# Performance work log

Hardware: AMD Instinct MI355X
Metric: run time of the kernel (lower is better)

The kernel has to match this reference:

```python
import jax, jax.numpy as jnp
import numpy as np
import math

B, S, E, H, L, VOCAB, OUT = 32, 1024, 512, 8, 2, 20000, 1
D = E // H


def positional_encoding(seq_length, embed_size):
    position = jnp.arange(seq_length, dtype=jnp.float32)[:, None]
    div_term = jnp.exp(jnp.arange(0, embed_size, 2, dtype=jnp.float32) * (-math.log(10000.0) / embed_size))
    pe = jnp.zeros((seq_length, embed_size), dtype=jnp.float32)
    pe = pe.at[:, 0::2].set(jnp.sin(position * div_term))
    pe = pe.at[:, 1::2].set(jnp.cos(position * div_term))
    return pe


def setup_inputs() -> dict:
    key = jax.random.key(0)
    ks = jax.random.split(key, 12)
    inputs = jax.random.randint(ks[0], (B, S), 0, VOCAB)
    s = 1.0 / math.sqrt(E)
    embed_table = jax.random.normal(ks[1], (VOCAB, E), jnp.float32)
    embed_table = embed_table.at[0].set(0.0)  # padding_idx=0
    # per-layer Q,K,V,O linear weights [L,E,E] (applied as x @ W + b) and biases [L,E]
    Wq = jax.random.normal(ks[2], (L, E, E), jnp.float32) * s
    Wk = jax.random.normal(ks[3], (L, E, E), jnp.float32) * s
    Wv = jax.random.normal(ks[4], (L, E, E), jnp.float32) * s
    Wo = jax.random.normal(ks[5], (L, E, E), jnp.float32) * s
    bq = jax.random.normal(ks[6], (L, E), jnp.float32) * s
    bk = jax.random.normal(ks[7], (L, E), jnp.float32) * s
    bv = jax.random.normal(ks[8], (L, E), jnp.float32) * s
    bo = jax.random.normal(ks[9], (L, E), jnp.float32) * s
    W_out = jax.random.normal(ks[10], (E, OUT), jnp.float32) * s
    b_out = jax.random.normal(ks[11], (OUT,), jnp.float32) * s
    return {"inputs": inputs, "embed_table": embed_table, "Wq": Wq, "bq": bq,
            "Wk": Wk, "bk": bk, "Wv": Wv, "bv": bv, "Wo": Wo, "bo": bo,
            "W_out": W_out, "b_out": b_out}


def _mha(x, Wq, bq, Wk, bk, Wv, bv, Wo, bo, mask):
    b, s = x.shape[:2]
    def heads(W, bias):
        return (x @ W + bias).reshape(b, s, H, D).transpose(0, 2, 1, 3)  # [b,H,s,D]
    q, k, v = heads(Wq, bq), heads(Wk, bk), heads(Wv, bv)
    scores = jnp.einsum('bhqd,bhkd->bhqk', q, k) / math.sqrt(D)
    scores = jnp.where(mask, -1e9, scores)
    prob = jax.nn.softmax(scores, axis=-1)
    out = jnp.einsum('bhqk,bhkd->bhqd', prob, v)
    out = out.transpose(0, 2, 1, 3).reshape(b, s, E)
    return out @ Wo + bo


def reference(inputs, embed_table, Wq, bq, Wk, bk, Wv, bv, Wo, bo, W_out, b_out):
    embeds = embed_table[inputs]  # [B,S,E]
    embeds = embeds + positional_encoding(inputs.shape[1], embeds.shape[-1])
    mask = jnp.triu(jnp.ones((inputs.shape[1], inputs.shape[1]), bool), k=1)  # future mask
    out = embeds
    for l in range(L):
        attn = _mha(out, Wq[l], bq[l], Wk[l], bk[l], Wv[l], bv[l], Wo[l], bo[l], mask)
        out = out + jax.nn.relu(attn)  # dropout is identity (eval / p=0)
    return out @ W_out + b_out
```

## Files before the change

kernel.cpp:

```cpp
#include <hip/hip_runtime.h>

typedef unsigned short u16;
typedef unsigned int u32;
using short8  = __attribute__((ext_vector_type(8))) short;
using floatx4 = __attribute__((ext_vector_type(4))) float;

#define NB 32
#define SEQ 1024
#define EMB 512
#define NH 8
#define HD 64
#define NLAYER 2
#define M_ROWS (NB * SEQ)

__device__ __forceinline__ float bf2f(u16 u) {
  union { u32 i; float f; } v; v.i = ((u32)u) << 16; return v.f;
}
__device__ __forceinline__ u16 f2bf(float f) {
  union { float f; u32 i; } v; v.f = f;
  u32 r = v.i + 0x7fffu + ((v.i >> 16) & 1u);
  return (u16)(r >> 16);
}
__device__ __forceinline__ u32 cvtpk(float a, float b) {
  u32 r;
  asm volatile("v_cvt_pk_bf16_f32 %0, %1, %2" : "=v"(r) : "v"(a), "v"(b));
  return r;
}

#if __has_builtin(__builtin_amdgcn_exp2f)
#define EXP2F __builtin_amdgcn_exp2f
#else
#define EXP2F exp2f
#endif

typedef __attribute__((address_space(3))) unsigned int lds_u32_t;
typedef __attribute__((address_space(1))) const unsigned int gbl_u32_t;
__device__ __forceinline__ void gload16(void* lds, const void* g) {
  gbl_u32_t* gp = (gbl_u32_t*)(unsigned long long)g;
  lds_u32_t* lp = (lds_u32_t*)(unsigned int)(unsigned long long)lds;
  __builtin_amdgcn_global_load_lds(gp, lp, 16, 0, 0);
}

__global__ void prep_weights(const float* __restrict__ Wq, const float* __restrict__ Wk,
                             const float* __restrict__ Wv, const float* __restrict__ Wo,
                             u16* __restrict__ WtQKV, u16* __restrict__ WtO) {
  int idx = blockIdx.x * 256 + threadIdx.x;
  const int QKV_TOT = NLAYER * 3 * EMB * EMB;
  if (idx < QKV_TOT) {
    int l = idx / (3 * EMB * EMB);
    int rem = idx % (3 * EMB * EMB);
    int n = rem / EMB, kk = rem % EMB;
    int w = n >> 9, e = n & 511;
    const float* src = (w == 0) ? Wq : (w == 1) ? Wk : Wv;
    WtQKV[idx] = f2bf(src[((size_t)l * EMB + kk) * EMB + e]);
  } else {
    int j = idx - QKV_TOT;
    int l = j / (EMB * EMB);
    int rem = j % (EMB * EMB);
    int n = rem / EMB, kk = rem % EMB;
    WtO[j] = f2bf(Wo[((size_t)l * EMB + kk) * EMB + n]);
  }
}

__global__ void pe_table(float* __restrict__ pe) {
  int idx = blockIdx.x * 256 + threadIdx.x;
  int s = idx >> 9, e = idx & 511;
  int i = e >> 1;
  const float negln = -9.210340371976184f / (float)EMB;
  float dt = __expf((float)(2 * i) * negln);
  float ang = (float)s * dt;
  pe[idx] = (e & 1) ? __cosf(ang) : __sinf(ang);
}

__global__ void embed_pe(const int* __restrict__ inp, const float* __restrict__ table,
                         const float* __restrict__ pe, u16* __restrict__ x) {
  int row = blockIdx.x;
  int tok = inp[row];
  int s = row & (SEQ - 1);
  int e = threadIdx.x * 2;
  float2 tv = *(const float2*)&table[(size_t)tok * EMB + e];
  float2 pv = *(const float2*)&pe[(size_t)s * EMB + e];
  *(u32*)&x[(size_t)row * EMB + e] = cvtpk(tv.x + pv.x, tv.y + pv.y);
}

#define BK 32

__global__ __launch_bounds__(256) void gemm_bt(
    const u16* __restrict__ A, const u16* __restrict__ Bt, int K, int mode,
    const float* bias0, const float* bias1, const float* bias2,
    u16* out0, u16* out1, u16* out2, const u16* resid, int Nstride) {
  __shared__ u16 sA[3][128][BK];
  __shared__ u16 sB[3][128][BK];
  int tid = threadIdx.x;
  int wave = tid >> 6, lane = tid & 63;
  int quad = lane >> 4, l16 = lane & 15;
  int wm = wave >> 1, wn = wave & 1;

  int NT = (mode == 0) ? 12 : 4;
  int blk = blockIdx.x;
  int xcd = blk & 7, slot = blk >> 3;
  int mtl = slot / NT, ntl = slot % NT;
  int bm0 = (xcd * 32 + mtl) * 128;
  int bn0 = ntl * 128;
  bool vswap = (mode == 0) && (bn0 >= 1024);

  floatx4 acc[4][4];
#pragma unroll
  for (int i = 0; i < 4; ++i)
#pragma unroll
    for (int j = 0; j < 4; ++j) acc[i][j] = (floatx4){0.f, 0.f, 0.f, 0.f};

  int rb = wave * 32;
  int lrow = lane >> 2;
  int gcg = ((lane & 3) ^ ((lane >> 3) & 3)) * 8;
  int rsl = (quad ^ ((l16 >> 1) & 3)) * 8;

  const u16* Arow0 = &A[(size_t)(bm0 + rb + lrow) * K + gcg];
  const u16* Arow1 = &A[(size_t)(bm0 + rb + 16 + lrow) * K + gcg];
  const u16* Brow0 = &Bt[(size_t)(bn0 + rb + lrow) * K + gcg];
  const u16* Brow1 = &Bt[(size_t)(bn0 + rb + 16 + lrow) * K + gcg];

  gload16(&sA[0][rb][0],      Arow0);
  gload16(&sA[0][rb + 16][0], Arow1);
  gload16(&sB[0][rb][0],      Brow0);
  gload16(&sB[0][rb + 16][0], Brow1);
  gload16(&sA[1][rb][0],      Arow0 + BK);
  gload16(&sA[1][rb + 16][0], Arow1 + BK);
  gload16(&sB[1][rb][0],      Brow0 + BK);
  gload16(&sB[1][rb + 16][0], Brow1 + BK);

  const int niter = K / BK;
  int c0 = 0, c1 = 1, c2 = 2;
  for (int it = 0; it < niter; ++it) {
    if (it + 2 < niter) {
      int k2 = (it + 2) * BK;
      gload16(&sA[c2][rb][0],      Arow0 + k2);
      gload16(&sA[c2][rb + 16][0], Arow1 + k2);
      gload16(&sB[c2][rb][0],      Brow0 + k2);
      gload16(&sB[c2][rb + 16][0], Brow1 + k2);
      asm volatile("s_waitcnt vmcnt(8)" ::: "memory");
    } else if (it + 1 < niter) {
      asm volatile("s_waitcnt vmcnt(4)" ::: "memory");
    } else {
      asm volatile("s_waitcnt vmcnt(0)" ::: "memory");
    }
    asm volatile("s_barrier" ::: "memory");

    short8 af[4], bfr[4];
#pragma unroll
    for (int mi = 0; mi < 4; ++mi)
      af[mi] = *(const short8*)&sA[c0][wm * 64 + mi * 16 + l16][rsl];
#pragma unroll
    for (int ni = 0; ni < 4; ++ni)
      bfr[ni] = *(const short8*)&sB[c0][wn * 64 + ni * 16 + l16][rsl];
    if (!vswap) {
#pragma unroll
      for (int mi = 0; mi < 4; ++mi)
#pragma unroll
        for (int ni = 0; ni < 4; ++ni)
          acc[mi][ni] = __builtin_amdgcn_mfma_f32_16x16x32_bf16(af[mi], bfr[ni], acc[mi][ni], 0, 0, 0);
    } else {
#pragma unroll
      for (int mi = 0; mi < 4; ++mi)
#pragma unroll
        for (int ni = 0; ni < 4; ++ni)
          acc[mi][ni] = __builtin_amdgcn_mfma_f32_16x16x32_bf16(bfr[ni], af[mi], acc[mi][ni], 0, 0, 0);
    }
    asm volatile("s_waitcnt lgkmcnt(0)" ::: "memory");
    asm volatile("s_barrier" ::: "memory");
    int t = c0; c0 = c1; c1 = c2; c2 = t;
  }

  u16* scr = ((u16*)sA) + wave * (16 * 68);
  int erow = lane >> 5;
  int dcol = lane & 31;

  if (!vswap) {
    int w = bn0 >> 9;
    const float* bp = (mode == 1) ? bias0 : ((w == 0) ? bias0 : bias1);
    float sc = (mode == 0 && w == 0) ? 0.18033688011112042f : 1.0f;
    float bvs[4];
#pragma unroll
    for (int ni = 0; ni < 4; ++ni)
      bvs[ni] = bp[(bn0 + wn * 64 + ni * 16 + l16) & 511] * sc;

    int colg = bn0 + wn * 64 + dcol * 2;
#pragma unroll
    for (int mi = 0; mi < 4; ++mi) {
#pragma unroll
      for (int ni = 0; ni < 4; ++ni) {
        float t0 = fmaf(acc[mi][ni][0], sc, bvs[ni]);
        float t1 = fmaf(acc[mi][ni][1], sc, bvs[ni]);
        float t2 = fmaf(acc[mi][ni][2], sc, bvs[ni]);
        float t3 = fmaf(acc[mi][ni][3], sc, bvs[ni]);
        if (mode == 1) {
          t0 = fmaxf(t0, 0.f); t1 = fmaxf(t1, 0.f);
          t2 = fmaxf(t2, 0.f); t3 = fmaxf(t3, 0.f);
        }
        u32 p01 = cvtpk(t0, t1), p23 = cvtpk(t2, t3);
        int base = (quad * 4) * 68 + ni * 16 + l16;
        scr[base]       = (u16)p01;
        scr[base + 68]  = (u16)(p01 >> 16);
        scr[base + 136] = (u16)p23;
        scr[base + 204] = (u16)(p23 >> 16);
      }
      asm volatile("s_waitcnt lgkmcnt(0)" ::: "memory");

      int m0 = bm0 + wm * 64 + mi * 16;
      if (mode == 0) {
        int e = colg & 511, hh = e >> 6, dd = e & 63;
        int bb = m0 >> 10, sid0 = m0 & 1023;
        u16* optr = (w == 0) ? out0 : out1;
        u16* op = &optr[((size_t)(bb * NH + hh) * SEQ + sid0) * HD + dd];
#pragma unroll
        for (int p = 0; p < 8; ++p) {
          int row = p * 2 + erow;
          u32 d2 = *(const u32*)&scr[row * 68 + dcol * 2];
          *(u32*)&op[(size_t)row * HD] = d2;
        }
      } else {
        size_t off0 = (size_t)m0 * Nstride + colg;
        const u16* rp = &resid[off0];
        u16* wp = &out0[off0];
#pragma unroll
        for (int p = 0; p < 8; ++p) {
          int row = p * 2 + erow;
          u32 d2 = *(const u32*)&scr[row * 68 + dcol * 2];
          u32 rs = *(const u32*)&rp[(size_t)row * Nstride];
          float lo = bf2f((u16)d2) + bf2f((u16)rs);
          float hi = bf2f((u16)(d2 >> 16)) + bf2f((u16)(rs >> 16));
          *(u32*)&wp[(size_t)row * Nstride] = cvtpk(lo, hi);
        }
      }
      asm volatile("s_waitcnt lgkmcnt(0)" ::: "memory");
    }
  } else {
    float bvv[4][4];
#pragma unroll
    for (int ni = 0; ni < 4; ++ni)
#pragma unroll
      for (int r = 0; r < 4; ++r)
        bvv[ni][r] = bias2[(bn0 + wn * 64 + ni * 16 + quad * 4 + r) & 511];

    int b = (bm0 + wm * 64) >> 10;
    int sid0 = (bm0 + wm * 64) & 1023;
    int n0 = bn0 + wn * 64;
    int h = (n0 >> 6) & 7;
#pragma unroll
    for (int ni = 0; ni < 4; ++ni) {
#pragma unroll
      for (int mi = 0; mi < 4; ++mi) {
        float t0 = acc[mi][ni][0] + bvv[ni][0];
        float t1 = acc[mi][ni][1] + bvv[ni][1];
        float t2 = acc[mi][ni][2] + bvv[ni][2];
        float t3 = acc[mi][ni][3] + bvv[ni][3];
        u32 p01 = cvtpk(t0, t1), p23 = cvtpk(t2, t3);
        int base = (quad * 4) * 68 + mi * 16 + l16;
        scr[base]       = (u16)p01;
        scr[base + 68]  = (u16)(p01 >> 16);
        scr[base + 136] = (u16)p23;
        scr[base + 204] = (u16)(p23 >> 16);
      }
      asm volatile("s_waitcnt lgkmcnt(0)" ::: "memory");

      int d0 = (n0 & 63) + ni * 16;
      u16* op2 = &out2[((size_t)(b * NH + h) * HD + d0) * SEQ + sid0 + dcol * 2];
#pragma unroll
      for (int p = 0; p < 8; ++p) {
        int row = p * 2 + erow;
        u32 d2 = *(const u32*)&scr[row * 68 + dcol * 2];
        *(u32*)&op2[(size_t)row * SEQ] = d2;
      }
      asm volatile("s_waitcnt lgkmcnt(0)" ::: "memory");
    }
  }
}

__device__ __forceinline__ void stage_tile64(u16 (*dst)[64], const u16* g, int gstride,
                                             int wave, int lane) {
  int r = lane >> 3;
  int gcg = ((lane & 7) ^ r) * 8;
#pragma unroll
  for (int c = 0; c < 2; ++c) {
    int row0 = (wave * 2 + c) * 8;
    gload16(&dst[row0][0], &g[(size_t)(row0 + r) * gstride + gcg]);
  }
}
#define RD8(T, row, cg) (*(const short8*)&T[row][(((cg) ^ ((row) & 7)) * 8)])

__global__ __launch_bounds__(256) void attn_kernel(
    const u16* __restrict__ q, const u16* __restrict__ k, const u16* __restrict__ vt,
    u16* __restrict__ o) {
  int blk = blockIdx.x;
  int xcd = blk & 7, slot = blk >> 3;
  int bh = xcd * 32 + (slot >> 2);
  int pr = slot & 3;
  int b = bh >> 3, h = bh & 7;
  __shared__ u16 sQ[128][64], sK[64][64], sV[64][64];
  __shared__ u16 sP[2][64][68];
  int tid = threadIdx.x, wave = tid >> 6, lane = tid & 63;
  int quad = lane >> 4, l16 = lane & 15;

  const u16* kbase = &k[(size_t)bh * SEQ * HD];
  const u16* vbase = &vt[(size_t)bh * HD * SEQ];

  short8 ones;
#pragma unroll
  for (int j = 0; j < 8; ++j) ones[j] = (short)0x3F80;

  for (int job = 0; job < 2; ++job) {
    int qtp = job ? (7 - pr) : pr;
    int qA0 = qtp * 128, qB0 = qA0 + 64;

    stage_tile64((u16(*)[64])&sQ[0][0],  &q[((size_t)bh * SEQ + qA0) * HD], HD, wave, lane);
    stage_tile64((u16(*)[64])&sQ[64][0], &q[((size_t)bh * SEQ + qB0) * HD], HD, wave, lane);

    floatx4 accoA[4], accoB[4], accsumA, accsumB;
#pragma unroll
    for (int i = 0; i < 4; ++i) {
      accoA[i] = (floatx4){0.f, 0.f, 0.f, 0.f};
      accoB[i] = (floatx4){0.f, 0.f, 0.f, 0.f};
    }
    accsumA = (floatx4){0.f, 0.f, 0.f, 0.f};
    accsumB = (floatx4){0.f, 0.f, 0.f, 0.f};
    short8 aqA0 = {}, aqA1 = {}, aqB0 = {}, aqB1 = {};

    auto process = [&](short8 aq0, short8 aq1, int qX0, bool diag, int sub,
                       floatx4* acco, floatx4& accsum, int k0) {
      floatx4 accs[4];
#pragma unroll
      for (int i = 0; i < 4; ++i) accs[i] = (floatx4){0.f, 0.f, 0.f, 0.f};
#pragma unroll
      for (int nt = 0; nt < 4; ++nt) {
        int rbk = nt * 16 + l16;
        accs[nt] = __builtin_amdgcn_mfma_f32_16x16x32_bf16(aq0, RD8(sK, rbk, quad), accs[nt], 0, 0, 0);
        accs[nt] = __builtin_amdgcn_mfma_f32_16x16x32_bf16(aq1, RD8(sK, rbk, 4 + quad), accs[nt], 0, 0, 0);
      }
      int prow = wave * 16 + quad * 4;
      if (!diag) {
#pragma unroll
        for (int nt = 0; nt < 4; ++nt)
#pragma unroll
          for (int r = 0; r < 4; ++r) {
            float p = EXP2F(fminf(accs[nt][r], 108.f));
            sP[sub][prow + r][nt * 16 + l16] = (u16)(__float_as_uint(p) >> 16);
          }
      } else {
        int qg_base = qX0 + prow;
#pragma unroll
        for (int nt = 0; nt < 4; ++nt) {
          int kg = k0 + nt * 16 + l16;
#pragma unroll
          for (int r = 0; r < 4; ++r) {
            float p = EXP2F(fminf(accs[nt][r], 108.f));
            if (kg > qg_base + r) p = 0.f;
            sP[sub][prow + r][nt * 16 + l16] = (u16)(__float_as_uint(p) >> 16);
          }
        }
      }
      asm volatile("s_waitcnt lgkmcnt(0)" ::: "memory");
#pragma unroll
      for (int cst = 0; cst < 2; ++cst) {
        short8 ap = *(const short8*)&sP[sub][wave * 16 + l16][cst * 32 + quad * 8];
#pragma unroll
        for (int dt = 0; dt < 4; ++dt) {
          int rv = dt * 16 + l16;
          acco[dt] = __builtin_amdgcn_mfma_f32_16x16x32_bf16(ap, RD8(sV, rv, cst * 4 + quad), acco[dt], 0, 0, 0);
        }
        accsum = __builtin_amdgcn_mfma_f32_16x16x32_bf16(ap, ones, accsum, 0, 0, 0);
      }
    };

    int ktmax = 2 * qtp + 1;
    for (int kt = 0; kt <= ktmax; ++kt) {
      int k0 = kt * 64;
      __syncthreads();
      stage_tile64(sK, &kbase[(size_t)k0 * HD], HD, wave, lane);
      stage_tile64(sV, &vbase[k0], SEQ, wave, lane);
      __syncthreads();

      if (kt == 0) {
        int ra = wave * 16 + l16;
        aqA0 = RD8(sQ, ra, quad);
        aqA1 = RD8(sQ, ra, 4 + quad);
        int rb_ = 64 + wave * 16 + l16;
        aqB0 = RD8(sQ, rb_, quad);
        aqB1 = RD8(sQ, rb_, 4 + quad);
      }

      if (kt <= 2 * qtp)
        process(aqA0, aqA1, qA0, kt == 2 * qtp, 0, accoA, accsumA, k0);
      process(aqB0, aqB1, qB0, kt == ktmax, 1, accoB, accsumB, k0);
    }

#pragma unroll
    for (int dt = 0; dt < 4; ++dt)
#pragma unroll
      for (int r = 0; r < 4; ++r) {
        int rowoff = wave * 16 + quad * 4 + r;
        int col = h * HD + dt * 16 + l16;
        o[((size_t)b * SEQ + qA0 + rowoff) * EMB + col] = f2bf(accoA[dt][r] / accsumA[r]);
        o[((size_t)b * SEQ + qB0 + rowoff) * EMB + col] = f2bf(accoB[dt][r] / accsumB[r]);
      }
  }
}

__global__ __launch_bounds__(256) void out_proj(const u16* __restrict__ x,
                                                const float* __restrict__ wout,
                                                const float* __restrict__ bout,
                                                float* __restrict__ out) {
  int wave = threadIdx.x >> 6, lane = threadIdx.x & 63;
  int m = blockIdx.x * 4 + wave;
  union { uint4 vv; u16 s[8]; } xv;
  xv.vv = *(const uint4*)&x[(size_t)m * EMB + lane * 8];
  float4 w0 = *(const float4*)&wout[lane * 8];
  float4 w1 = *(const float4*)&wout[lane * 8 + 4];
  float wv[8] = {w0.x, w0.y, w0.z, w0.w, w1.x, w1.y, w1.z, w1.w};
  float s = 0.f;
#pragma unroll
  for (int j = 0; j < 8; ++j) s += bf2f(xv.s[j]) * wv[j];
#pragma unroll
  for (int sh = 1; sh < 64; sh <<= 1) s += __shfl_xor(s, sh, 64);
  if (lane == 0) out[m] = s + bout[0];
}

extern "C" void kernel_launch(void* const* d_in, const int* in_sizes, int n_in,
                              void* d_out, int out_size, void* d_ws, size_t ws_size,
                              hipStream_t stream) {
  const int*   inp   = (const int*)d_in[0];
  const float* table = (const float*)d_in[1];
  const float* Wq    = (const float*)d_in[2];
  const float* bq    = (const float*)d_in[3];
  const float* Wk    = (const float*)d_in[4];
  const float* bk    = (const float*)d_in[5];
  const float* Wv    = (const float*)d_in[6];
  const float* bv    = (const float*)d_in[7];
  const float* Wo    = (const float*)d_in[8];
  const float* bo    = (const float*)d_in[9];
  const float* Wout  = (const float*)d_in[10];
  const float* bout  = (const float*)d_in[11];
  float* outp = (float*)d_out;

  char* ws = (char*)d_ws;
  const size_t SZ = (size_t)M_ROWS * EMB * 2;
  u16* x      = (u16*)(ws);
  u16* qb     = (u16*)(ws + SZ);
  u16* kb     = (u16*)(ws + 2 * SZ);
  u16* vb     = (u16*)(ws + 3 * SZ);
  u16* attn_b = (u16*)(ws + 4 * SZ);
  u16* WtQKV  = (u16*)(ws + 5 * SZ);
  u16* WtO    = (u16*)(ws + 5 * SZ + (size_t)NLAYER * 3 * EMB * EMB * 2);
  float* pe   = (float*)(ws + 5 * SZ + (size_t)NLAYER * 4 * EMB * EMB * 2);

  prep_weights<<<8192, 256, 0, stream>>>(Wq, Wk, Wv, Wo, WtQKV, WtO);
  pe_table<<<2048, 256, 0, stream>>>(pe);
  embed_pe<<<M_ROWS, 256, 0, stream>>>(inp, table, pe, x);

  for (int l = 0; l < NLAYER; ++l) {
    gemm_bt<<<3072, 256, 0, stream>>>(
        x, WtQKV + (size_t)l * 3 * EMB * EMB, EMB, 0,
        bq + l * EMB, bk + l * EMB, bv + l * EMB, qb, kb, vb, nullptr, 0);
    attn_kernel<<<1024, 256, 0, stream>>>(qb, kb, vb, attn_b);
    gemm_bt<<<1024, 256, 0, stream>>>(
        attn_b, WtO + (size_t)l * EMB * EMB, EMB, 1,
        bo + l * EMB, nullptr, nullptr, x, nullptr, nullptr, x, EMB);
  }
  out_proj<<<8192, 256, 0, stream>>>(x, Wout, bout, outp);
}
```

Before: 564.0 us.

## Give each wave private LDS tiles in GEMM to remove block barriers

```diff
diff --git a/kernel.cpp b/kernel.cpp
--- a/kernel.cpp
+++ b/kernel.cpp
@@ -89,8 +89,7 @@
     const u16* __restrict__ A, const u16* __restrict__ Bt, int K, int mode,
     const float* bias0, const float* bias1, const float* bias2,
     u16* out0, u16* out1, u16* out2, const u16* resid, int Nstride) {
-  __shared__ u16 sA[3][128][BK];
-  __shared__ u16 sB[3][128][BK];
+  __shared__ u16 smem[4][2][2][64][BK];
   int tid = threadIdx.x;
   int wave = tid >> 6, lane = tid & 63;
   int quad = lane >> 4, l16 = lane & 15;
@@ -110,49 +109,43 @@
 #pragma unroll
     for (int j = 0; j < 4; ++j) acc[i][j] = (floatx4){0.f, 0.f, 0.f, 0.f};
 
-  int rb = wave * 32;
   int lrow = lane >> 2;
   int gcg = ((lane & 3) ^ ((lane >> 3) & 3)) * 8;
   int rsl = (quad ^ ((l16 >> 1) & 3)) * 8;
 
-  const u16* Arow0 = &A[(size_t)(bm0 + rb + lrow) * K + gcg];
-  const u16* Arow1 = &A[(size_t)(bm0 + rb + 16 + lrow) * K + gcg];
-  const u16* Brow0 = &Bt[(size_t)(bn0 + rb + lrow) * K + gcg];
-  const u16* Brow1 = &Bt[(size_t)(bn0 + rb + 16 + lrow) * K + gcg];
-
-  gload16(&sA[0][rb][0],      Arow0);
-  gload16(&sA[0][rb + 16][0], Arow1);
-  gload16(&sB[0][rb][0],      Brow0);
-  gload16(&sB[0][rb + 16][0], Brow1);
-  gload16(&sA[1][rb][0],      Arow0 + BK);
-  gload16(&sA[1][rb + 16][0], Arow1 + BK);
-  gload16(&sB[1][rb][0],      Brow0 + BK);
-  gload16(&sB[1][rb + 16][0], Brow1 + BK);
-
+  const u16* Arp[4];
+  const u16* Brp[4];
+#pragma unroll
+  for (int g = 0; g < 4; ++g) {
+    Arp[g] = &A [(size_t)(bm0 + wm * 64 + g * 16 + lrow) * K + gcg];
+    Brp[g] = &Bt[(size_t)(bn0 + wn * 64 + g * 16 + lrow) * K + gcg];
+  }
+
+  auto stage = [&](int buf, int kk) {
+#pragma unroll
+    for (int g = 0; g < 4; ++g) {
+      gload16(&smem[wave][buf][0][g * 16][0], Arp[g] + kk);
+      gload16(&smem[wave][buf][1][g * 16][0], Brp[g] + kk);
+    }
+  };
+
+  stage(0, 0);
   const int niter = K / BK;
-  int c0 = 0, c1 = 1, c2 = 2;
   for (int it = 0; it < niter; ++it) {
-    if (it + 2 < niter) {
-      int k2 = (it + 2) * BK;
-      gload16(&sA[c2][rb][0],      Arow0 + k2);
-      gload16(&sA[c2][rb + 16][0], Arow1 + k2);
-      gload16(&sB[c2][rb][0],      Brow0 + k2);
-      gload16(&sB[c2][rb + 16][0], Brow1 + k2);
+    if (it + 1 < niter) {
+      stage((it + 1) & 1, (it + 1) * BK);
       asm volatile("s_waitcnt vmcnt(8)" ::: "memory");
-    } else if (it + 1 < niter) {
-      asm volatile("s_waitcnt vmcnt(4)" ::: "memory");
     } else {
       asm volatile("s_waitcnt vmcnt(0)" ::: "memory");
     }
-    asm volatile("s_barrier" ::: "memory");
-
+    int c = it & 1;
     short8 af[4], bfr[4];
 #pragma unroll
     for (int mi = 0; mi < 4; ++mi)
-      af[mi] = *(const short8*)&sA[c0][wm * 64 + mi * 16 + l16][rsl];
+      af[mi] = *(const short8*)&smem[wave][c][0][mi * 16 + l16][rsl];
 #pragma unroll
     for (int ni = 0; ni < 4; ++ni)
-      bfr[ni] = *(const short8*)&sB[c0][wn * 64 + ni * 16 + l16][rsl];
+      bfr[ni] = *(const short8*)&smem[wave][c][1][ni * 16 + l16][rsl];
     if (!vswap) {
 #pragma unroll
       for (int mi = 0; mi < 4; ++mi)
@@ -166,12 +159,9 @@
         for (int ni = 0; ni < 4; ++ni)
           acc[mi][ni] = __builtin_amdgcn_mfma_f32_16x16x32_bf16(bfr[ni], af[mi], acc[mi][ni], 0, 0, 0);
     }
-    asm volatile("s_waitcnt lgkmcnt(0)" ::: "memory");
-    asm volatile("s_barrier" ::: "memory");
-    int t = c0; c0 = c1; c1 = c2; c2 = t;
-  }
-
-  u16* scr = ((u16*)sA) + wave * (16 * 68);
+  }
+
+  u16* scr = (u16*)&smem[wave][0][0][0][0];
   int erow = lane >> 5;
   int dcol = lane & 31;
 
```

After: 582.0 us. +3.2%, slower.

## Fuse paired causal query jobs into one KV sweep sharing K/V tiles

Applied to the files above, without the earlier changes.

```diff
diff --git a/kernel.cpp b/kernel.cpp
--- a/kernel.cpp
+++ b/kernel.cpp
@@ -296,113 +296,123 @@
   int bh = xcd * 32 + (slot >> 2);
   int pr = slot & 3;
   int b = bh >> 3, h = bh & 7;
-  __shared__ u16 sQ[128][64], sK[64][64], sV[64][64];
-  __shared__ u16 sP[2][64][68];
+  int qS = pr, qL = 7 - pr;
+  int sA0 = qS * 128, sB0 = sA0 + 64;
+  int lA0 = qL * 128, lB0 = lA0 + 64;
+  __shared__ u16 sK[64][64], sV[64][64];
+  __shared__ u16 sP[4][64][68];
   int tid = threadIdx.x, wave = tid >> 6, lane = tid & 63;
   int quad = lane >> 4, l16 = lane & 15;
 
   const u16* kbase = &k[(size_t)bh * SEQ * HD];
   const u16* vbase = &vt[(size_t)bh * HD * SEQ];
 
+  int qrow = wave * 16 + l16;
+  const u16* qb_ = &q[((size_t)bh * SEQ + qrow) * HD + quad * 8];
+  short8 aqSA0 = *(const short8*)&qb_[(size_t)sA0 * HD];
+  short8 aqSA1 = *(const short8*)&qb_[(size_t)sA0 * HD + 32];
+  short8 aqSB0 = *(const short8*)&qb_[(size_t)sB0 * HD];
+  short8 aqSB1 = *(const short8*)&qb_[(size_t)sB0 * HD + 32];
+  short8 aqLA0 = *(const short8*)&qb_[(size_t)lA0 * HD];
+  short8 aqLA1 = *(const short8*)&qb_[(size_t)lA0 * HD + 32];
+  short8 aqLB0 = *(const short8*)&qb_[(size_t)lB0 * HD];
+  short8 aqLB1 = *(const short8*)&qb_[(size_t)lB0 * HD + 32];
+
   short8 ones;
 #pragma unroll
   for (int j = 0; j < 8; ++j) ones[j] = (short)0x3F80;
 
-  for (int job = 0; job < 2; ++job) {
-    int qtp = job ? (7 - pr) : pr;
-    int qA0 = qtp * 128, qB0 = qA0 + 64;
-
-    stage_tile64((u16(*)[64])&sQ[0][0],  &q[((size_t)bh * SEQ + qA0) * HD], HD, wave, lane);
-    stage_tile64((u16(*)[64])&sQ[64][0], &q[((size_t)bh * SEQ + qB0) * HD], HD, wave, lane);
-
-    floatx4 accoA[4], accoB[4], accsumA, accsumB;
-#pragma unroll
-    for (int i = 0; i < 4; ++i) {
-      accoA[i] = (floatx4){0.f, 0.f, 0.f, 0.f};
-      accoB[i] = (floatx4){0.f, 0.f, 0.f, 0.f};
-    }
-    accsumA = (floatx4){0.f, 0.f, 0.f, 0.f};
-    accsumB = (floatx4){0.f, 0.f, 0.f, 0.f};
-    short8 aqA0 = {}, aqA1 = {}, aqB0 = {}, aqB1 = {};
-
-    auto process = [&](short8 aq0, short8 aq1, int qX0, bool diag, int sub,
-                       floatx4* acco, floatx4& accsum, int k0) {
-      floatx4 accs[4];
-#pragma unroll
-      for (int i = 0; i < 4; ++i) accs[i] = (floatx4){0.f, 0.f, 0.f, 0.f};
+  floatx4 accSA[4], accSB[4], accLA[4], accLB[4];
+  floatx4 sumSA, sumSB, sumLA, sumLB;
+#pragma unroll
+  for (int i = 0; i < 4; ++i) {
+    accSA[i] = (floatx4){0.f, 0.f, 0.f, 0.f};
+    accSB[i] = (floatx4){0.f, 0.f, 0.f, 0.f};
+    accLA[i] = (floatx4){0.f, 0.f, 0.f, 0.f};
+    accLB[i] = (floatx4){0.f, 0.f, 0.f, 0.f};
+  }
+  sumSA = (floatx4){0.f, 0.f, 0.f, 0.f};
+  sumSB = (floatx4){0.f, 0.f, 0.f, 0.f};
+  sumLA = (floatx4){0.f, 0.f, 0.f, 0.f};
+  sumLB = (floatx4){0.f, 0.f, 0.f, 0.f};
+
+  auto process = [&](short8 aq0, short8 aq1, int qX0, bool diag, int slotP,
+                     floatx4* acco, floatx4& accsum, int k0) {
+    floatx4 accs[4];
+#pragma unroll
+    for (int i = 0; i < 4; ++i) accs[i] = (floatx4){0.f, 0.f, 0.f, 0.f};
+#pragma unroll
+    for (int nt = 0; nt < 4; ++nt) {
+      int rbk = nt * 16 + l16;
+      accs[nt] = __builtin_amdgcn_mfma_f32_16x16x32_bf16(aq0, RD8(sK, rbk, quad), accs[nt], 0, 0, 0);
+      accs[nt] = __builtin_amdgcn_mfma_f32_16x16x32_bf16(aq1, RD8(sK, rbk, 4 + quad), accs[nt], 0, 0, 0);
+    }
+    int prow = wave * 16 + quad * 4;
+    if (!diag) {
+#pragma unroll
+      for (int nt = 0; nt < 4; ++nt)
+#pragma unroll
+        for (int r = 0; r < 4; ++r) {
+          float p = EXP2F(fminf(accs[nt][r], 108.f));
+          sP[slotP][prow + r][nt * 16 + l16] = (u16)(__float_as_uint(p) >> 16);
+        }
+    } else {
+      int qg_base = qX0 + prow;
 #pragma unroll
       for (int nt = 0; nt < 4; ++nt) {
-        int rbk = nt * 16 + l16;
-        accs[nt] = __builtin_amdgcn_mfma_f32_16x16x32_bf16(aq0, RD8(sK, rbk, quad), accs[nt], 0, 0, 0);
-        accs[nt] = __builtin_amdgcn_mfma_f32_16x16x32_bf16(aq1, RD8(sK, rbk, 4 + quad), accs[nt], 0, 0, 0);
-      }
-      int prow = wave * 16 + quad * 4;
-      if (!diag) {
-#pragma unroll
-        for (int nt = 0; nt < 4; ++nt)
-#pragma unroll
-          for (int r = 0; r < 4; ++r) {
-            float p = EXP2F(fminf(accs[nt][r], 108.f));
-            sP[sub][prow + r][nt * 16 + l16] = (u16)(__float_as_uint(p) >> 16);
-          }
-      } else {
-        int qg_base = qX0 + prow;
-#pragma unroll
-        for (int nt = 0; nt < 4; ++nt) {
-          int kg = k0 + nt * 16 + l16;
-#pragma unroll
-          for (int r = 0; r < 4; ++r) {
-            float p = EXP2F(fminf(accs[nt][r], 108.f));
-            if (kg > qg_base + r) p = 0.f;
-            sP[sub][prow + r][nt * 16 + l16] = (u16)(__float_as_uint(p) >> 16);
-          }
+        int kg = k0 + nt * 16 + l16;
+#pragma unroll
+        for (int r = 0; r < 4; ++r) {
+          float p = EXP2F(fminf(accs[nt][r], 108.f));
+          if (kg > qg_base + r) p = 0.f;
+          sP[slotP][prow + r][nt * 16 + l16] = (u16)(__float_as_uint(p) >> 16);
         }
       }
-      asm volatile("s_waitcnt lgkmcnt(0)" ::: "memory");
-#pragma unroll
-      for (int cst = 0; cst < 2; ++cst) {
-        short8 ap = *(const short8*)&sP[sub][wave * 16 + l16][cst * 32 + quad * 8];
-#pragma unroll
-        for (int dt = 0; dt < 4; ++dt) {
-          int rv = dt * 16 + l16;
-          acco[dt] = __builtin_amdgcn_mfma_f32_16x16x32_bf16(ap, RD8(sV, rv, cst * 4 + quad), acco[dt], 0, 0, 0);
-        }
-        accsum = __builtin_amdgcn_mfma_f32_16x16x32_bf16(ap, ones, accsum, 0, 0, 0);
-      }
-    };
-
-    int ktmax = 2 * qtp + 1;
-    for (int kt = 0; kt <= ktmax; ++kt) {
-      int k0 = kt * 64;
-      __syncthreads();
-      stage_tile64(sK, &kbase[(size_t)k0 * HD], HD, wave, lane);
-      stage_tile64(sV, &vbase[k0], SEQ, wave, lane);
-      __syncthreads();
-
-      if (kt == 0) {
-        int ra = wave * 16 + l16;
-        aqA0 = RD8(sQ, ra, quad);
-        aqA1 = RD8(sQ, ra, 4 + quad);
-        int rb_ = 64 + wave * 16 + l16;
-        aqB0 = RD8(sQ, rb_, quad);
-        aqB1 = RD8(sQ, rb_, 4 + quad);
-      }
-
-      if (kt <= 2 * qtp)
-        process(aqA0, aqA1, qA0, kt == 2 * qtp, 0, accoA, accsumA, k0);
-      process(aqB0, aqB1, qB0, kt == ktmax, 1, accoB, accsumB, k0);
-    }
-
+    }
+    asm volatile("s_waitcnt lgkmcnt(0)" ::: "memory");
+#pragma unroll
+    for (int cst = 0; cst < 2; ++cst) {
+      short8 ap = *(const short8*)&sP[slotP][wave * 16 + l16][cst * 32 + quad * 8];
+#pragma unroll
+      for (int dt = 0; dt < 4; ++dt) {
+        int rv = dt * 16 + l16;
+        acco[dt] = __builtin_amdgcn_mfma_f32_16x16x32_bf16(ap, RD8(sV, rv, cst * 4 + quad), acco[dt], 0, 0, 0);
+      }
+      accsum = __builtin_amdgcn_mfma_f32_16x16x32_bf16(ap, ones, accsum, 0, 0, 0);
+    }
+  };
+
+  int ktmaxL = 2 * qL + 1;
+  for (int kt = 0; kt <= ktmaxL; ++kt) {
+    int k0 = kt * 64;
+    __syncthreads();
+    stage_tile64(sK, &kbase[(size_t)k0 * HD], HD, wave, lane);
+    stage_tile64(sV, &vbase[k0], SEQ, wave, lane);
+    __syncthreads();
+
+    if (kt <= 2 * qS)
+      process(aqSA0, aqSA1, sA0, kt == 2 * qS, 0, accSA, sumSA, k0);
+    if (kt <= 2 * qS + 1)
+      process(aqSB0, aqSB1, sB0, kt == 2 * qS + 1, 1, accSB, sumSB, k0);
+    if (kt <= 2 * qL)
+      process(aqLA0, aqLA1, lA0, kt == 2 * qL, 2, accLA, sumLA, k0);
+    process(aqLB0, aqLB1, lB0, kt == ktmaxL, 3, accLB, sumLB, k0);
+  }
+
+  auto writeo = [&](int base, floatx4* acco, floatx4& accsum) {
 #pragma unroll
     for (int dt = 0; dt < 4; ++dt)
 #pragma unroll
       for (int r = 0; r < 4; ++r) {
         int rowoff = wave * 16 + quad * 4 + r;
         int col = h * HD + dt * 16 + l16;
-        o[((size_t)b * SEQ + qA0 + rowoff) * EMB + col] = f2bf(accoA[dt][r] / accsumA[r]);
-        o[((size_t)b * SEQ + qB0 + rowoff) * EMB + col] = f2bf(accoB[dt][r] / accsumB[r]);
-      }
-  }
+        o[((size_t)b * SEQ + base + rowoff) * EMB + col] = f2bf(acco[dt][r] / accsum[r]);
+      }
+  };
+  writeo(sA0, accSA, sumSA);
+  writeo(sB0, accSB, sumSB);
+  writeo(lA0, accLA, sumLA);
+  writeo(lB0, accLB, sumLB);
 }
 
 __global__ __launch_bounds__(256) void out_proj(const u16* __restrict__ x,
```

After: 572.3 us. About the same (+1.5%).
